# Optimization experiments

Hardware: AMD Instinct MI355X
Metric: run time of the kernel (lower is better)

The kernel has to match this reference:

```python
import jax, jax.numpy as jnp
import numpy as np

REPEAT_STEP = 4  # speculative_num_draft_tokens


def setup_inputs() -> dict:
    key = jax.random.key(0)
    k1, k2, k3, k4, k5 = jax.random.split(key, 5)
    BS = 512
    M = BS * REPEAT_STEP          # 2048 expanded rows
    LEN_A = 16384
    LEN_B = 128
    LEN_OUT = LEN_A + LEN_B
    return {
        "page_table_dst": jax.random.randint(k1, (M, LEN_OUT), 0, 1000000, dtype=jnp.int32),
        "page_table_a": jax.random.randint(k2, (BS, LEN_A), 0, 1000000, dtype=jnp.int32),
        "page_table_b": jax.random.randint(k3, (M, LEN_B), 0, 1000000, dtype=jnp.int32),
        "seq_len_a": jax.random.randint(k4, (BS,), 0, LEN_A, dtype=jnp.int32),
        "seq_len_b": jax.random.randint(k5, (M,), 0, LEN_B, dtype=jnp.int32),
    }


def reference(page_table_dst, page_table_a, page_table_b, seq_len_a, seq_len_b):
    M, LEN_OUT = page_table_dst.shape
    LEN_A = page_table_a.shape[1]
    LEN_B = page_table_b.shape[1]

    idx_a = jnp.arange(M) // REPEAT_STEP            # [M] map expanded row -> base row
    sa = seq_len_a[idx_a][:, None]                  # [M,1]
    sb = seq_len_b[:, None]                         # [M,1]
    offs = jnp.arange(LEN_OUT)[None, :]             # [1,LEN_OUT]

    # source-A values: gather the base row, valid where offs < seq_len_a (and in bounds)
    a_rows = page_table_a[idx_a]                    # [M, LEN_A]
    a_idx = jnp.broadcast_to(jnp.clip(offs, 0, LEN_A - 1), (M, LEN_OUT))
    a_val = jnp.take_along_axis(a_rows, a_idx, axis=1)
    a_val = jnp.where((offs < sa) & (offs < LEN_A), a_val, 0)

    # source-B values: shifted by seq_len_a per row
    b_offs = offs - sa                              # [M,LEN_OUT]
    b_idx = jnp.clip(b_offs, 0, LEN_B - 1)
    b_val = jnp.take_along_axis(page_table_b, b_idx, axis=1)
    b_val = jnp.where((b_offs >= 0) & (b_offs < sb) & (b_offs < LEN_B), b_val, 0)

    spliced = jnp.where(offs < sa, a_val, b_val)
    total = sa + sb
    # positions beyond total_len keep the original dst contents (kernel masks stores)
    return jnp.where(offs < total, spliced, page_table_dst)
```

## Files before the change

### kernel.cpp

```cpp
#include <hip/hip_runtime.h>


__global__ __launch_bounds__(256) void splice_kernel(
    const int* __restrict__ dst,
    const int* __restrict__ a,
    const int* __restrict__ b,
    const int* __restrict__ seq_a,
    const int* __restrict__ seq_b,
    int* __restrict__ out,
    int LEN_OUT, int LEN_A, int LEN_B, int repeat_shift)
{
    const int m  = blockIdx.y;
    const int vc = blockIdx.x * blockDim.x + threadIdx.x;
    const int nvec = LEN_OUT >> 2;
    if (vc >= nvec) return;

    const int ia    = m >> repeat_shift;
    const int sa    = seq_a[ia];
    const int sb    = seq_b[m];
    const int total = sa + sb;
    const int j0    = vc << 2;

    const int* a_row   = a   + (size_t)ia * LEN_A;
    const int* dst_row = dst + (size_t)m  * LEN_OUT;

    int4 v;
    if (j0 + 3 < sa) {
        v = *(const int4*)(a_row + j0);
    } else if (j0 >= total) {
        v = *(const int4*)(dst_row + j0);
    } else {
        const int* b_row = b + (size_t)m * LEN_B;
        int vals[4];
#pragma unroll
        for (int k = 0; k < 4; ++k) {
            const int j = j0 + k;
            int val;
            if (j < sa)         val = a_row[j];
            else if (j < total) val = b_row[j - sa];
            else                val = dst_row[j];
            vals[k] = val;
        }
        v = make_int4(vals[0], vals[1], vals[2], vals[3]);
    }
    *(int4*)(out + (size_t)m * LEN_OUT + j0) = v;
}

extern "C" void kernel_launch(void* const* d_in, const int* in_sizes, int n_in,
                              void* d_out, int out_size, void* d_ws, size_t ws_size,
                              hipStream_t stream) {
    const int* dst   = (const int*)d_in[0];
    const int* a     = (const int*)d_in[1];
    const int* b     = (const int*)d_in[2];
    const int* seq_a = (const int*)d_in[3];
    const int* seq_b = (const int*)d_in[4];
    int* out = (int*)d_out;

    const int BS      = in_sizes[3];
    const int M       = in_sizes[4];
    const int LEN_A   = in_sizes[1] / BS;
    const int LEN_B   = in_sizes[2] / M;
    const int LEN_OUT = in_sizes[0] / M;
    const int repeat  = M / BS;
    int repeat_shift = 0;
    while ((1 << repeat_shift) < repeat) ++repeat_shift;

    const int nvec = LEN_OUT / 4;
    dim3 block(256);
    dim3 grid((nvec + 255) / 256, M);
    splice_kernel<<<grid, block, 0, stream>>>(dst, a, b, seq_a, seq_b, out,
                                              LEN_OUT, LEN_A, LEN_B, repeat_shift);
}
```

Before: 247.4 us.

## Use one block per row with a strided loop and nontemporal loads/stores

Changes the grid from a 2D tiling (chunks by rows) to one 256-thread block per output row that loops over the row in 1024-int strides with unroll 4. Per-row seq lengths and row pointers are computed once per block, and the int4 branching is expressed in vector-index thresholds. Destination reads and output writes use nontemporal builtins to avoid polluting cache with streaming data. The risk is fewer blocks in flight (2048 blocks, each doing ~16 iterations), which may reduce memory-level parallelism per CU.

```diff
diff --git a/kernel.cpp b/kernel.cpp
--- a/kernel.cpp
+++ b/kernel.cpp
@@ -1,5 +1,28 @@
 #include <hip/hip_runtime.h>
 
+
+typedef int v4i __attribute__((ext_vector_type(4)));
+
+__device__ __forceinline__ v4i splice_vec(
+    int vc, int sa, int total, int nA, int nTail,
+    const int* __restrict__ a_row, const int* __restrict__ b_row,
+    const int* __restrict__ dst_row)
+{
+    const int j0 = vc << 2;
+    if (vc < nA) {
+        return *(const v4i*)(a_row + j0);
+    } else if (vc >= nTail) {
+        return __builtin_nontemporal_load((const v4i*)(dst_row + j0));
+    } else {
+        v4i v;
+#pragma unroll
+        for (int t = 0; t < 4; ++t) {
+            const int j = j0 + t;
+            v[t] = (j < sa) ? a_row[j] : ((j < total) ? b_row[j - sa] : dst_row[j]);
+        }
+        return v;
+    }
+}
 
 __global__ __launch_bounds__(256) void splice_kernel(
     const int* __restrict__ dst,
@@ -10,40 +33,34 @@
     int* __restrict__ out,
     int LEN_OUT, int LEN_A, int LEN_B, int repeat_shift)
 {
-    const int m  = blockIdx.y;
-    const int vc = blockIdx.x * blockDim.x + threadIdx.x;
-    const int nvec = LEN_OUT >> 2;
-    if (vc >= nvec) return;
+    const int m   = blockIdx.x;
+    const int tid = threadIdx.x;
 
     const int ia    = m >> repeat_shift;
     const int sa    = seq_a[ia];
     const int sb    = seq_b[m];
     const int total = sa + sb;
-    const int j0    = vc << 2;
+    const int nvec  = LEN_OUT >> 2;
+    const int nA    = sa >> 2;
+    const int nTail = (total + 3) >> 2;
 
     const int* a_row   = a   + (size_t)ia * LEN_A;
+    const int* b_row   = b   + (size_t)m  * LEN_B;
     const int* dst_row = dst + (size_t)m  * LEN_OUT;
+    int*       out_row = out + (size_t)m  * LEN_OUT;
 
-    int4 v;
-    if (j0 + 3 < sa) {
-        v = *(const int4*)(a_row + j0);
-    } else if (j0 >= total) {
-        v = *(const int4*)(dst_row + j0);
-    } else {
-        const int* b_row = b + (size_t)m * LEN_B;
-        int vals[4];
-#pragma unroll
-        for (int k = 0; k < 4; ++k) {
-            const int j = j0 + k;
-            int val;
-            if (j < sa)         val = a_row[j];
-            else if (j < total) val = b_row[j - sa];
-            else                val = dst_row[j];
-            vals[k] = val;
-        }
-        v = make_int4(vals[0], vals[1], vals[2], vals[3]);
+    const int full = nvec >> 8;
+#pragma unroll 4
+    for (int k = 0; k < full; ++k) {
+        const int vc = (k << 8) + tid;
+        v4i v = splice_vec(vc, sa, total, nA, nTail, a_row, b_row, dst_row);
+        __builtin_nontemporal_store(v, (v4i*)(out_row + (vc << 2)));
     }
-    *(int4*)(out + (size_t)m * LEN_OUT + j0) = v;
+    const int vc = (full << 8) + tid;
+    if (vc < nvec) {
+        v4i v = splice_vec(vc, sa, total, nA, nTail, a_row, b_row, dst_row);
+        __builtin_nontemporal_store(v, (v4i*)(out_row + (vc << 2)));
+    }
 }
 
 extern "C" void kernel_launch(void* const* d_in, const int* in_sizes, int n_in,
@@ -65,9 +82,6 @@
     int repeat_shift = 0;
     while ((1 << repeat_shift) < repeat) ++repeat_shift;
 
-    const int nvec = LEN_OUT / 4;
-    dim3 block(256);
-    dim3 grid((nvec + 255) / 256, M);
-    splice_kernel<<<grid, block, 0, stream>>>(dst, a, b, seq_a, seq_b, out,
-                                              LEN_OUT, LEN_A, LEN_B, repeat_shift);
+    splice_kernel<<<dim3(M), dim3(256), 0, stream>>>(dst, a, b, seq_a, seq_b, out,
+                                                     LEN_OUT, LEN_A, LEN_B, repeat_shift);
 }
```

Result: no change. 252.2 us (+1.9%).
